# Optimization experiments

Hardware: AMD Instinct MI355X
Metric: run time of the kernel (lower is better)

## Reference

```python
import jax, jax.numpy as jnp
import numpy as np

INITIAL_DELTA = 0.1
DELTA_LOW = 0.02
DELTA_HIGH = 0.1
SCAN_LEN_OFFSET = 20  # scan over num_columns - 20
EXTRA_LO, EXTRA_HI = 232, 252  # pass-through columns


def setup_inputs() -> dict:
    key = jax.random.key(0)
    x = jax.random.normal(key, (128, 1024, 252), dtype=jnp.float32)
    return {"x": x}


def _delta_modulate(x):
    # x: [B, R, C]; scan over first C-20 columns with per-(b,r) state.
    B, R, C = x.shape
    n_steps = C - SCAN_LEN_OFFSET
    xs = jnp.moveaxis(x[:, :, :n_steps], -1, 0)  # [n_steps, B, R]

    dc0 = jnp.zeros((B, R), dtype=x.dtype)
    delta0 = jnp.full((B, R), INITIAL_DELTA, dtype=x.dtype)
    tc0 = jnp.zeros((B, R), dtype=x.dtype)
    ntc0 = jnp.zeros((B, R), dtype=x.dtype)

    def step(carry, x_i):
        dc, delta, tc, ntc = carry
        up = x_i > (dc + delta)
        dn = x_i < (dc - delta)
        trig = up | dn
        tc = jnp.where(trig, tc + 1.0, 0.0)
        ntc = jnp.where(trig, 0.0, ntc + 1.0)
        delta = jnp.where(tc >= 3.0, DELTA_LOW, delta)
        delta = jnp.where(ntc >= 3.0, DELTA_HIGH, delta)
        dc = jnp.where(trig, x_i, dc)
        return (dc, delta, tc, ntc), (up, dn)

    _, (UP, DN) = jax.lax.scan(step, (dc0, delta0, tc0, ntc0), xs)
    # UP/DN: [n_steps, B, R] bool -> [B, R, n_steps]
    UP = jnp.moveaxis(UP, 0, -1)
    DN = jnp.moveaxis(DN, 0, -1)
    encoded = jnp.concatenate([UP, DN], axis=-1).astype(jnp.float32)
    extra = x[:, :, EXTRA_LO:EXTRA_HI]
    return jnp.concatenate([encoded, extra], axis=-1).astype(jnp.float32)


def reference(x) -> jnp.ndarray:
    return _delta_modulate(x)
```

## Files before the change

kernel.cpp:

```cpp
#include <hip/hip_runtime.h>

#define CC 252
#define NSTEPS 232
#define OUTC 484
#define NROWS (128 * 1024)
#define ROWS_PER_BLOCK 256

#define INITIAL_DELTA 0.1f
#define DELTA_LOW 0.02f
#define DELTA_HIGH 0.1f

#define BITS_STRIDE 17
#define EXTRA_STRIDE 21

template<int NV>
__device__ __forceinline__ void scan_vecs(const float4* xv, unsigned& uw, unsigned& dw,
                                          float& dc, float& delta, float& tc, float& ntc)
{
    uw = 0u; dw = 0u;
    #pragma unroll
    for (int k = 0; k < NV; ++k) {
        float xs[4] = {xv[k].x, xv[k].y, xv[k].z, xv[k].w};
        #pragma unroll
        for (int j = 0; j < 4; ++j) {
            float xi = xs[j];
            bool up = xi > dc + delta;
            bool dn = xi < dc - delta;
            bool trig = up || dn;
            tc  = trig ? tc + 1.0f : 0.0f;
            ntc = trig ? 0.0f : ntc + 1.0f;
            delta = (tc  >= 3.0f) ? DELTA_LOW  : delta;
            delta = (ntc >= 3.0f) ? DELTA_HIGH : delta;
            dc = trig ? xi : dc;
            uw |= (up ? 1u : 0u) << (k * 4 + j);
            dw |= (dn ? 1u : 0u) << (k * 4 + j);
        }
    }
}

#define PREFETCH8(buf, base) { \
    _Pragma("unroll") for (int k = 0; k < 8; ++k) buf[k] = x4[(base) + k]; }

__global__ __launch_bounds__(256) void DeltaModulator_kernel(
    const float* __restrict__ x, float* __restrict__ out)
{
    __shared__ unsigned bits_lds[ROWS_PER_BLOCK * BITS_STRIDE];
    __shared__ float    extra_lds[ROWS_PER_BLOCK * EXTRA_STRIDE];

    const int t = threadIdx.x;
    const int row0 = blockIdx.x * ROWS_PER_BLOCK;

    {
        const int row = row0 + t;
        const float* xrow = x + (size_t)row * CC;
        const float4* __restrict__ x4 = reinterpret_cast<const float4*>(xrow);

        float dc = 0.0f, delta = INITIAL_DELTA, tc = 0.0f, ntc = 0.0f;
        unsigned* __restrict__ myb = &bits_lds[t * BITS_STRIDE];
        unsigned uw, dw;

        float4 bA[8], bB[8];

        PREFETCH8(bA, 0);
        PREFETCH8(bB, 8);
        scan_vecs<8>(bA, uw, dw, dc, delta, tc, ntc);
        myb[0] = uw; myb[8] = dw;

        PREFETCH8(bA, 16);
        scan_vecs<8>(bB, uw, dw, dc, delta, tc, ntc);
        myb[1] = uw; myb[9] = dw;

        PREFETCH8(bB, 24);
        scan_vecs<8>(bA, uw, dw, dc, delta, tc, ntc);
        myb[2] = uw; myb[10] = dw;

        PREFETCH8(bA, 32);
        scan_vecs<8>(bB, uw, dw, dc, delta, tc, ntc);
        myb[3] = uw; myb[11] = dw;

        PREFETCH8(bB, 40);
        scan_vecs<8>(bA, uw, dw, dc, delta, tc, ntc);
        myb[4] = uw; myb[12] = dw;

        PREFETCH8(bA, 48);
        scan_vecs<8>(bB, uw, dw, dc, delta, tc, ntc);
        myb[5] = uw; myb[13] = dw;

        {
            #pragma unroll
            for (int k = 0; k < 7; ++k) bB[k] = x4[56 + k];
        }
        scan_vecs<8>(bA, uw, dw, dc, delta, tc, ntc);
        myb[6] = uw; myb[14] = dw;

        scan_vecs<2>(bB, uw, dw, dc, delta, tc, ntc);
        myb[7] = uw; myb[15] = dw;

        {
            float* __restrict__ mye = &extra_lds[t * EXTRA_STRIDE];
            #pragma unroll
            for (int i = 0; i < 5; ++i) {
                float4 v = bB[2 + i];
                mye[i * 4 + 0] = v.x;
                mye[i * 4 + 1] = v.y;
                mye[i * 4 + 2] = v.z;
                mye[i * 4 + 3] = v.w;
            }
        }
    }

    __syncthreads();

    float4* __restrict__ o4 = reinterpret_cast<float4*>(out + (size_t)row0 * OUTC);

    int r = (t >= 242) ? 2 : ((t >= 121) ? 1 : 0);
    int f = t - r * 121;

    #pragma unroll 1
    for (int i = 0; i < 121; ++i) {
        float4 v;
        if (f < 116) {
            const int idx   = (f < 58) ? f : f - 58;
            const int wbase = (f < 58) ? 0 : 8;
            const unsigned word = bits_lds[r * BITS_STRIDE + wbase + (idx >> 3)];
            const int s = 4 * (idx & 7);
            v = make_float4((float)((word >> s) & 1u),
                            (float)((word >> (s + 1)) & 1u),
                            (float)((word >> (s + 2)) & 1u),
                            (float)((word >> (s + 3)) & 1u));
        } else {
            const float* e = &extra_lds[r * EXTRA_STRIDE + (f - 116) * 4];
            v = make_float4(e[0], e[1], e[2], e[3]);
        }
        o4[r * 121 + f] = v;

        f += 14; r += 2;
        if (f >= 121) { f -= 121; r += 1; }
    }
}

extern "C" void kernel_launch(void* const* d_in, const int* in_sizes, int n_in,
                              void* d_out, int out_size, void* d_ws, size_t ws_size,
                              hipStream_t stream) {
    const float* x = (const float*)d_in[0];
    float* out = (float*)d_out;
    const int threads = 256;
    const int blocks = NROWS / ROWS_PER_BLOCK;
    DeltaModulator_kernel<<<blocks, threads, 0, stream>>>(x, out);
}
```

Before: 358.2 us.

## Coalesce input loads via cooperative LDS staging transpose per chunk

Each thread previously read its own row with strided float4 loads, so lanes touched addresses about 1 KB apart. Now groups of 8 threads load 8 consecutive float4s of a row together and stage the chunk through shared memory, after which each thread reads its own row back for the serial scan. The pass-through columns are served from the last staged chunk instead of a separate buffer. This adds two barriers per chunk and more LDS use, which may lower occupancy, in exchange for better-coalesced global reads.

```diff
diff --git a/kernel.cpp b/kernel.cpp
--- a/kernel.cpp
+++ b/kernel.cpp
@@ -5,13 +5,14 @@
 #define OUTC 484
 #define NROWS (128 * 1024)
 #define ROWS_PER_BLOCK 256
+#define ROW_F4 63
 
 #define INITIAL_DELTA 0.1f
 #define DELTA_LOW 0.02f
 #define DELTA_HIGH 0.1f
 
+#define STG 11
 #define BITS_STRIDE 17
-#define EXTRA_STRIDE 21
 
 template<int NV>
 __device__ __forceinline__ void scan_vecs(const float4* xv, unsigned& uw, unsigned& dw,
@@ -38,74 +39,60 @@
     }
 }
 
-#define PREFETCH8(buf, base) { \
-    _Pragma("unroll") for (int k = 0; k < 8; ++k) buf[k] = x4[(base) + k]; }
-
 __global__ __launch_bounds__(256) void DeltaModulator_kernel(
     const float* __restrict__ x, float* __restrict__ out)
 {
+    __shared__ float4   stage[ROWS_PER_BLOCK * STG];
     __shared__ unsigned bits_lds[ROWS_PER_BLOCK * BITS_STRIDE];
-    __shared__ float    extra_lds[ROWS_PER_BLOCK * EXTRA_STRIDE];
 
     const int t = threadIdx.x;
     const int row0 = blockIdx.x * ROWS_PER_BLOCK;
+    const int rsub = t >> 3;
+    const int v    = t & 7;
 
-    {
-        const int row = row0 + t;
-        const float* xrow = x + (size_t)row * CC;
-        const float4* __restrict__ x4 = reinterpret_cast<const float4*>(xrow);
+    const float4* __restrict__ xb =
+        reinterpret_cast<const float4*>(x) + (size_t)row0 * ROW_F4;
 
-        float dc = 0.0f, delta = INITIAL_DELTA, tc = 0.0f, ntc = 0.0f;
-        unsigned* __restrict__ myb = &bits_lds[t * BITS_STRIDE];
+    float dc = 0.0f, delta = INITIAL_DELTA, tc = 0.0f, ntc = 0.0f;
+    unsigned* __restrict__ myb = &bits_lds[t * BITS_STRIDE];
+
+    float4 greg[8], rowreg[8];
+
+    #pragma unroll
+    for (int i = 0; i < 8; ++i)
+        greg[i] = xb[(size_t)(i * 32 + rsub) * ROW_F4 + v];
+
+    #pragma unroll
+    for (int ch = 0; ch < 8; ++ch) {
+        __syncthreads();
+        #pragma unroll
+        for (int i = 0; i < 8; ++i)
+            stage[(i * 32 + rsub) * STG + v] = greg[i];
+        __syncthreads();
+
+        #pragma unroll
+        for (int k = 0; k < 8; ++k)
+            rowreg[k] = stage[t * STG + k];
+
+        if (ch < 6) {
+            #pragma unroll
+            for (int i = 0; i < 8; ++i)
+                greg[i] = xb[(size_t)(i * 32 + rsub) * ROW_F4 + (ch + 1) * 8 + v];
+        } else if (ch == 6) {
+            if (v < 7) {
+                #pragma unroll
+                for (int i = 0; i < 8; ++i)
+                    greg[i] = xb[(size_t)(i * 32 + rsub) * ROW_F4 + 56 + v];
+            }
+        }
+
         unsigned uw, dw;
-
-        float4 bA[8], bB[8];
-
-        PREFETCH8(bA, 0);
-        PREFETCH8(bB, 8);
-        scan_vecs<8>(bA, uw, dw, dc, delta, tc, ntc);
-        myb[0] = uw; myb[8] = dw;
-
-        PREFETCH8(bA, 16);
-        scan_vecs<8>(bB, uw, dw, dc, delta, tc, ntc);
-        myb[1] = uw; myb[9] = dw;
-
-        PREFETCH8(bB, 24);
-        scan_vecs<8>(bA, uw, dw, dc, delta, tc, ntc);
-        myb[2] = uw; myb[10] = dw;
-
-        PREFETCH8(bA, 32);
-        scan_vecs<8>(bB, uw, dw, dc, delta, tc, ntc);
-        myb[3] = uw; myb[11] = dw;
-
-        PREFETCH8(bB, 40);
-        scan_vecs<8>(bA, uw, dw, dc, delta, tc, ntc);
-        myb[4] = uw; myb[12] = dw;
-
-        PREFETCH8(bA, 48);
-        scan_vecs<8>(bB, uw, dw, dc, delta, tc, ntc);
-        myb[5] = uw; myb[13] = dw;
-
-        {
-            #pragma unroll
-            for (int k = 0; k < 7; ++k) bB[k] = x4[56 + k];
-        }
-        scan_vecs<8>(bA, uw, dw, dc, delta, tc, ntc);
-        myb[6] = uw; myb[14] = dw;
-
-        scan_vecs<2>(bB, uw, dw, dc, delta, tc, ntc);
-        myb[7] = uw; myb[15] = dw;
-
-        {
-            float* __restrict__ mye = &extra_lds[t * EXTRA_STRIDE];
-            #pragma unroll
-            for (int i = 0; i < 5; ++i) {
-                float4 v = bB[2 + i];
-                mye[i * 4 + 0] = v.x;
-                mye[i * 4 + 1] = v.y;
-                mye[i * 4 + 2] = v.z;
-                mye[i * 4 + 3] = v.w;
-            }
+        if (ch < 7) {
+            scan_vecs<8>(rowreg, uw, dw, dc, delta, tc, ntc);
+            myb[ch] = uw;  myb[8 + ch] = dw;
+        } else {
+            scan_vecs<2>(rowreg, uw, dw, dc, delta, tc, ntc);
+            myb[7] = uw;   myb[15] = dw;
         }
     }
 
@@ -118,21 +105,20 @@
 
     #pragma unroll 1
     for (int i = 0; i < 121; ++i) {
-        float4 v;
+        float4 w;
         if (f < 116) {
             const int idx   = (f < 58) ? f : f - 58;
             const int wbase = (f < 58) ? 0 : 8;
             const unsigned word = bits_lds[r * BITS_STRIDE + wbase + (idx >> 3)];
             const int s = 4 * (idx & 7);
-            v = make_float4((float)((word >> s) & 1u),
+            w = make_float4((float)((word >> s) & 1u),
                             (float)((word >> (s + 1)) & 1u),
                             (float)((word >> (s + 2)) & 1u),
                             (float)((word >> (s + 3)) & 1u));
         } else {
-            const float* e = &extra_lds[r * EXTRA_STRIDE + (f - 116) * 4];
-            v = make_float4(e[0], e[1], e[2], e[3]);
+            w = stage[r * STG + 2 + (f - 116)];
         }
-        o4[r * 121 + f] = v;
+        o4[r * 121 + f] = w;
 
         f += 14; r += 2;
         if (f >= 121) { f -= 121; r += 1; }
```

New measurement: 387.8 us. 1.08x slower.
